# Optimization experiments

Measured on AMD Instinct MI355X. Metric: run time of the kernel, lower is better.

Reference implementation:

```python
import jax, jax.numpy as jnp
import numpy as np

B, C, H, W = 8, 256, 160, 160

def setup_inputs() -> dict:
    key = jax.random.key(0)
    kx, kw, kh = jax.random.split(key, 3)
    x = jax.random.normal(kx, (B, C, H, W), dtype=jnp.float32)
    # kaiming_normal fan_in, relu -> std = sqrt(2/fan_in)
    fcw_w = jax.random.normal(kw, (1, W), dtype=jnp.float32) * np.float32(np.sqrt(2.0 / W))
    fch_w = jax.random.normal(kh, (1, H), dtype=jnp.float32) * np.float32(np.sqrt(2.0 / H))
    fcw_b = jnp.zeros((1,), dtype=jnp.float32)
    fch_b = jnp.zeros((1,), dtype=jnp.float32)
    return {"x": x, "fcw_w": fcw_w, "fcw_b": fcw_b, "fch_w": fch_w, "fch_b": fch_b}

def reference(x, fcw_w, fcw_b, fch_w, fch_b):
    b, c, h, w = x.shape
    xr = x.reshape(b * c, h, w)                                   # (n,h,w)
    # fc_w: Linear(w,1) then softmax over h (dim=1 of (n,h,1))
    alpha = jax.nn.softmax(jnp.einsum('nhw,w->nh', xr, fcw_w[0]) + fcw_b[0], axis=1)  # (n,h)
    # repeat+bmm == broadcasting a softmax-weighted row-sum to every row:
    # x_c[n,i,:] = sum_h alpha[n,h] * x[n,h,:]  (same for all i)
    row = jnp.einsum('nh,nhw->nw', alpha, xr)                      # (n,w)
    # fc_h on x_c^T (n,w,h): each h-column of x_c^T equals row, so the
    # Linear(h,1) reduces to row * sum(fch_w) + bias (identical math)
    beta = jax.nn.softmax(row * jnp.sum(fch_w[0]) + fch_b[0], axis=1)  # (n,w)
    # second repeat+bmm collapses to a scalar per (b,c): sum_w beta*row
    s = jnp.einsum('nw,nw->n', beta, row)                          # (n,)
    out = jnp.broadcast_to(s[:, None, None], (b * c, h, w)).reshape(b, c, h, w)
    return out
```

## Files before the change

kernel.cpp:

```cpp
#include <hip/hip_runtime.h>


#define HH 160
#define WW 160
#define NPLANE (HH * WW)
#define BLOCK 320
#define RPT 20
#define QN 40
#define PSTR 41

typedef float f32x4 __attribute__((ext_vector_type(4)));

__global__ void __launch_bounds__(BLOCK, 4) sa1_reduce(
    const float* __restrict__ x,
    const float* __restrict__ fcw_w,
    const float* __restrict__ fch_w,
    float* __restrict__ s_out)
{
    const int n = blockIdx.x;
    const int t = threadIdx.x;
    const int q = t % QN;
    const int v = t / QN;

    __shared__ float pbuf[HH * PSTR];
    __shared__ float larrA[HH];
    __shared__ float larrB[HH];
    __shared__ float sc[4];

    const float* xp = x + (size_t)n * NPLANE;

    const float4 ww = *(const float4*)(fcw_w + 4 * q);

    f32x4 xr[RPT];
#pragma unroll
    for (int r = 0; r < RPT; ++r)
        xr[r] = __builtin_nontemporal_load(
            (const f32x4*)(xp + (size_t)(v * RPT + r) * WW + 4 * q));
#pragma unroll
    for (int r = 0; r < RPT; ++r) {
        float p = xr[r].x * ww.x + xr[r].y * ww.y + xr[r].z * ww.z + xr[r].w * ww.w;
        pbuf[(v * RPT + r) * PSTR + q] = p;
    }
    __syncthreads();

    {
        const int h = (t < HH) ? t : (t - HH);
        const int qb = (t < HH) ? 0 : (QN / 2);
        const float* pr = pbuf + h * PSTR + qb;
        float s0 = 0.f, s1 = 0.f, s2 = 0.f, s3 = 0.f;
#pragma unroll
        for (int qq = 0; qq < QN / 2; qq += 4) {
            s0 += pr[qq]; s1 += pr[qq + 1]; s2 += pr[qq + 2]; s3 += pr[qq + 3];
        }
        float hs = (s0 + s1) + (s2 + s3);
        if (t < HH) larrA[h] = hs; else larrB[h] = hs;
    }
    __syncthreads();

    if (t < 32) {
        float lv[5];
#pragma unroll
        for (int j = 0; j < 5; ++j) lv[j] = larrA[t + 32 * j] + larrB[t + 32 * j];
        float m = lv[0];
#pragma unroll
        for (int j = 1; j < 5; ++j) m = fmaxf(m, lv[j]);
#pragma unroll
        for (int off = 16; off >= 1; off >>= 1)
            m = fmaxf(m, __shfl_down(m, off, 32));
        m = __shfl(m, 0, 32);
        float z = 0.f;
#pragma unroll
        for (int j = 0; j < 5; ++j) z += __expf(lv[j] - m);
#pragma unroll
        for (int off = 16; off >= 1; off >>= 1)
            z += __shfl_down(z, off, 32);
        if (t == 0) { sc[0] = m; sc[1] = z; }
    } else if (t >= 64 && t < 96) {
        const int u = t - 64;
        float s = 0.f;
#pragma unroll
        for (int j = 0; j < 5; ++j) s += fch_w[u + 32 * j];
#pragma unroll
        for (int off = 16; off >= 1; off >>= 1)
            s += __shfl_down(s, off, 32);
        if (u == 0) sc[2] = s;
    }
    __syncthreads();

    const float m = sc[0];
    float4 rp = make_float4(0.f, 0.f, 0.f, 0.f);
#pragma unroll
    for (int r = 0; r < RPT; ++r) {
        const int h = v * RPT + r;
        const float a = __expf((larrA[h] + larrB[h]) - m);
        rp.x += a * xr[r].x; rp.y += a * xr[r].y;
        rp.z += a * xr[r].z; rp.w += a * xr[r].w;
    }
    *(float4*)(pbuf + v * WW + 4 * q) = rp;
    __syncthreads();

    if (t < 32) {
        const float S = sc[2];
        const float rcpZ = 1.0f / sc[1];
        float rv[5], bl[5];
#pragma unroll
        for (int j = 0; j < 5; ++j) {
            const int w = t + 32 * j;
            float rs = 0.f;
#pragma unroll
            for (int vv = 0; vv < 8; ++vv) rs += pbuf[vv * WW + w];
            rv[j] = rs * rcpZ;
            bl[j] = rv[j] * S;
        }
        float mb = bl[0];
#pragma unroll
        for (int j = 1; j < 5; ++j) mb = fmaxf(mb, bl[j]);
#pragma unroll
        for (int off = 16; off >= 1; off >>= 1)
            mb = fmaxf(mb, __shfl_down(mb, off, 32));
        mb = __shfl(mb, 0, 32);
        float zb = 0.f, sd = 0.f;
#pragma unroll
        for (int j = 0; j < 5; ++j) {
            float e = __expf(bl[j] - mb);
            zb += e; sd += e * rv[j];
        }
#pragma unroll
        for (int off = 16; off >= 1; off >>= 1) {
            zb += __shfl_down(zb, off, 32);
            sd += __shfl_down(sd, off, 32);
        }
        if (t == 0) s_out[n] = sd / zb;
    }
}

#define BBLK 256
#define BIT (NPLANE / 4 / BBLK)

__global__ void __launch_bounds__(BBLK) sa1_bcast(
    const float* __restrict__ s, float* __restrict__ out)
{
    const int n = blockIdx.x;
    const float sv = s[n];
    const f32x4 o = { sv, sv, sv, sv };
    float* op = out + (size_t)n * NPLANE;
#pragma unroll
    for (int i = 0; i < BIT; ++i)
        __builtin_nontemporal_store(
            o, (f32x4*)(op + 4 * (size_t)(i * BBLK + threadIdx.x)));
}

extern "C" void kernel_launch(void* const* d_in, const int* in_sizes, int n_in,
                              void* d_out, int out_size, void* d_ws, size_t ws_size,
                              hipStream_t stream) {
    const float* x     = (const float*)d_in[0];
    const float* fcw_w = (const float*)d_in[1];
    const float* fch_w = (const float*)d_in[3];
    float* out = (float*)d_out;
    float* svec = (float*)d_ws;

    const int nplanes = 8 * 256;
    sa1_reduce<<<nplanes, BLOCK, 0, stream>>>(x, fcw_w, fch_w, svec);
    sa1_bcast<<<nplanes, BBLK, 0, stream>>>(svec, out);
}
```

Measured before the change: 345.2 us.

## Split each plane's reduction across two blocks with online-softmax merge in broadcast kernel

The reduction kernel now gives each plane to two blocks, each covering 80 rows. Each block writes a partial weighted row sum plus its softmax max and sum to workspace. The broadcast kernel merges the two halves with log-sum-exp rescaling, computes the second softmax, and writes the output, so the separate s-vector step disappears. The aim is more blocks and higher occupancy (fewer registers per thread, launch bound 7) for the read-bound reduction. The cost is extra workspace traffic and a fallback path when the workspace is too small.

```diff
diff --git a/kernel.cpp b/kernel.cpp
--- a/kernel.cpp
+++ b/kernel.cpp
@@ -5,11 +5,175 @@
 #define WW 160
 #define NPLANE (HH * WW)
 #define BLOCK 320
-#define RPT 20
 #define QN 40
 #define PSTR 41
 
+#define HALF 80
+#define RPTH 10
+#define WSSTR 164
+
 typedef float f32x4 __attribute__((ext_vector_type(4)));
+
+__global__ void __launch_bounds__(BLOCK, 7) sa1_part(
+    const float* __restrict__ x,
+    const float* __restrict__ fcw_w,
+    float* __restrict__ ws)
+{
+    const int bid = blockIdx.x;
+    const int n = bid >> 1;
+    const int g = bid & 1;
+    const int t = threadIdx.x;
+    const int q = t % QN;
+    const int v = t / QN;
+
+    __shared__ float pbuf[HALF * PSTR];
+    __shared__ float larr[HALF];
+    __shared__ float sc[2];
+
+    const float* xp = x + (size_t)n * NPLANE + (size_t)g * HALF * WW;
+
+    const float4 ww = *(const float4*)(fcw_w + 4 * q);
+
+    f32x4 xr[RPTH];
+#pragma unroll
+    for (int r = 0; r < RPTH; ++r)
+        xr[r] = __builtin_nontemporal_load(
+            (const f32x4*)(xp + (size_t)(v * RPTH + r) * WW + 4 * q));
+#pragma unroll
+    for (int r = 0; r < RPTH; ++r) {
+        float p = xr[r].x * ww.x + xr[r].y * ww.y + xr[r].z * ww.z + xr[r].w * ww.w;
+        pbuf[(v * RPTH + r) * PSTR + q] = p;
+    }
+    __syncthreads();
+
+    {
+        const int row = t >> 2;
+        const int seg = t & 3;
+        const float* pr = pbuf + row * PSTR + seg * 10;
+        float s0 = 0.f, s1 = 0.f;
+#pragma unroll
+        for (int i = 0; i < 10; i += 2) { s0 += pr[i]; s1 += pr[i + 1]; }
+        float hs = s0 + s1;
+        hs += __shfl_xor(hs, 1, 64);
+        hs += __shfl_xor(hs, 2, 64);
+        if (seg == 0) larr[row] = hs;
+    }
+    __syncthreads();
+
+    if (t < 32) {
+        const float l0 = larr[t];
+        const float l1 = larr[t + 32];
+        const float l2 = (t < 16) ? larr[t + 64] : -3.0e38f;
+        float m = fmaxf(l0, fmaxf(l1, l2));
+#pragma unroll
+        for (int off = 16; off >= 1; off >>= 1)
+            m = fmaxf(m, __shfl_down(m, off, 32));
+        m = __shfl(m, 0, 32);
+        float z = __expf(l0 - m) + __expf(l1 - m) + __expf(l2 - m);
+#pragma unroll
+        for (int off = 16; off >= 1; off >>= 1)
+            z += __shfl_down(z, off, 32);
+        if (t == 0) { sc[0] = m; sc[1] = z; }
+    }
+    __syncthreads();
+
+    const float m = sc[0];
+    float4 rp = make_float4(0.f, 0.f, 0.f, 0.f);
+#pragma unroll
+    for (int r = 0; r < RPTH; ++r) {
+        const float a = __expf(larr[v * RPTH + r] - m);
+        rp.x += a * xr[r].x; rp.y += a * xr[r].y;
+        rp.z += a * xr[r].z; rp.w += a * xr[r].w;
+    }
+    *(float4*)(pbuf + v * WW + 4 * q) = rp;
+    __syncthreads();
+
+    float* wsr = ws + (size_t)bid * WSSTR;
+    if (t < WW) {
+        float rs = 0.f;
+#pragma unroll
+        for (int vv = 0; vv < 8; ++vv) rs += pbuf[vv * WW + t];
+        wsr[t] = rs;
+    }
+    if (t == 0) { wsr[160] = sc[0]; wsr[161] = sc[1]; }
+}
+
+#define BBLK 256
+#define BIT (NPLANE / 4 / BBLK)
+
+__global__ void __launch_bounds__(BBLK) sa1_bcast_merge(
+    const float* __restrict__ ws,
+    const float* __restrict__ fch_w,
+    float* __restrict__ out)
+{
+    const int n = blockIdx.x;
+    const int t = threadIdx.x;
+    __shared__ float sc[2];
+
+    float rv[5];
+    if (t < 32) {
+        const float* r0 = ws + (size_t)(2 * n) * WSSTR;
+        const float* r1 = ws + (size_t)(2 * n + 1) * WSSTR;
+        const float m0 = r0[160], z0 = r0[161];
+        const float m1 = r1[160], z1 = r1[161];
+        const float mm = fmaxf(m0, m1);
+        const float f0 = __expf(m0 - mm);
+        const float f1 = __expf(m1 - mm);
+        const float rcpZ = 1.0f / (f0 * z0 + f1 * z1);
+#pragma unroll
+        for (int j = 0; j < 5; ++j) {
+            const int w = t + 32 * j;
+            rv[j] = (f0 * r0[w] + f1 * r1[w]) * rcpZ;
+        }
+    } else if (t >= 64 && t < 96) {
+        const int u = t - 64;
+        float s = 0.f;
+#pragma unroll
+        for (int j = 0; j < 5; ++j) s += fch_w[u + 32 * j];
+#pragma unroll
+        for (int off = 16; off >= 1; off >>= 1)
+            s += __shfl_down(s, off, 32);
+        if (u == 0) sc[0] = s;
+    }
+    __syncthreads();
+
+    if (t < 32) {
+        const float S = sc[0];
+        float bl[5];
+#pragma unroll
+        for (int j = 0; j < 5; ++j) bl[j] = rv[j] * S;
+        float mb = bl[0];
+#pragma unroll
+        for (int j = 1; j < 5; ++j) mb = fmaxf(mb, bl[j]);
+#pragma unroll
+        for (int off = 16; off >= 1; off >>= 1)
+            mb = fmaxf(mb, __shfl_down(mb, off, 32));
+        mb = __shfl(mb, 0, 32);
+        float zb = 0.f, sd = 0.f;
+#pragma unroll
+        for (int j = 0; j < 5; ++j) {
+            float e = __expf(bl[j] - mb);
+            zb += e; sd += e * rv[j];
+        }
+#pragma unroll
+        for (int off = 16; off >= 1; off >>= 1) {
+            zb += __shfl_down(zb, off, 32);
+            sd += __shfl_down(sd, off, 32);
+        }
+        if (t == 0) sc[1] = sd / zb;
+    }
+    __syncthreads();
+
+    const float sv = sc[1];
+    const f32x4 o = { sv, sv, sv, sv };
+    float* op = out + (size_t)n * NPLANE;
+#pragma unroll
+    for (int i = 0; i < BIT; ++i)
+        __builtin_nontemporal_store(
+            o, (f32x4*)(op + 4 * (size_t)(i * BBLK + threadIdx.x)));
+}
+
+#define RPT 20
 
 __global__ void __launch_bounds__(BLOCK, 4) sa1_reduce(
     const float* __restrict__ x,
@@ -28,7 +192,6 @@
     __shared__ float sc[4];
 
     const float* xp = x + (size_t)n * NPLANE;
-
     const float4 ww = *(const float4*)(fcw_w + 4 * q);
 
     f32x4 xr[RPT];
@@ -133,9 +296,6 @@
         if (t == 0) s_out[n] = sd / zb;
     }
 }
-
-#define BBLK 256
-#define BIT (NPLANE / 4 / BBLK)
 
 __global__ void __launch_bounds__(BBLK) sa1_bcast(
     const float* __restrict__ s, float* __restrict__ out)
@@ -157,9 +317,17 @@
     const float* fcw_w = (const float*)d_in[1];
     const float* fch_w = (const float*)d_in[3];
     float* out = (float*)d_out;
-    float* svec = (float*)d_ws;
 
     const int nplanes = 8 * 256;
-    sa1_reduce<<<nplanes, BLOCK, 0, stream>>>(x, fcw_w, fch_w, svec);
-    sa1_bcast<<<nplanes, BBLK, 0, stream>>>(svec, out);
-}
+    const size_t need = (size_t)(2 * nplanes) * WSSTR * sizeof(float);
+
+    if (ws_size >= need) {
+        float* wsp = (float*)d_ws;
+        sa1_part<<<2 * nplanes, BLOCK, 0, stream>>>(x, fcw_w, wsp);
+        sa1_bcast_merge<<<nplanes, BBLK, 0, stream>>>(wsp, fch_w, out);
+    } else {
+        float* svec = (float*)d_ws;
+        sa1_reduce<<<nplanes, BLOCK, 0, stream>>>(x, fcw_w, fch_w, svec);
+        sa1_bcast<<<nplanes, BBLK, 0, stream>>>(svec, out);
+    }
+}
```

After: 341.5 us (median of 2 runs). About the same (-1.1%).
